# Kernel optimization log

Hardware: AMD Instinct MI355X
Metric: run time of the kernel (lower is better)

Reference implementation:

```python
import jax, jax.numpy as jnp
import numpy as np

DIM, HID, BATCH = 64, 512, 8192


def setup_inputs() -> dict:
    key = jax.random.key(0)
    ks = jax.random.split(key, 6)
    s1 = 1.0 / np.sqrt(DIM + 1)
    s2 = 1.0 / np.sqrt(HID)
    return {
        "t": jax.random.uniform(ks[0], (1,), dtype=jnp.float32),
        "x": jax.random.normal(ks[1], (BATCH, DIM), dtype=jnp.float32),
        "W1": jax.random.normal(ks[2], (DIM + 1, HID), dtype=jnp.float32) * s1,
        "b1": jnp.zeros((HID,), jnp.float32),
        "W2": jax.random.normal(ks[3], (HID, HID), dtype=jnp.float32) * s2,
        "b2": jnp.zeros((HID,), jnp.float32),
        "W3": jax.random.normal(ks[4], (HID, DIM), dtype=jnp.float32) * s2,
        "b3": jnp.zeros((DIM,), jnp.float32),
    }


def _vf_single(ts, xs, W1, b1, W2, b2, W3, b3):
    # xs: [dim], ts: scalar. Time concatenated as extra input feature.
    h = jnp.concatenate([xs, ts[None]])          # [dim+1]
    h = jnp.tanh(h @ W1 + b1)                    # [hid]
    h = jnp.tanh(h @ W2 + b2)                    # [hid]
    return h @ W3 + b3                           # [dim]


def reference(t, x, W1, b1, W2, b2, W3, b3):
    ts = t[0]
    vf = lambda xs: _vf_single(ts, xs, W1, b1, W2, b2, W3, b3)
    v = jax.vmap(vf)(x)                                   # [B, dim]
    # Exact divergence: trace of per-sample Jacobian dv/dx.
    # (Replaces the torch per-dim autograd.grad loop with one batched jacfwd.)
    J = jax.vmap(jax.jacfwd(vf))(x)                       # [B, dim, dim]
    div = jnp.trace(J, axis1=-2, axis2=-1)                # [B]
    return (v, -div[:, None])
```

## Files before the change

kernel.cpp:

```cpp
#include <hip/hip_runtime.h>

#define DIM 64
#define HID 512
#define BATCH 8192
#define MB 32
#define NTHR 1024

typedef __attribute__((ext_vector_type(8))) short short8;
typedef __attribute__((ext_vector_type(4))) float f32x4;
typedef __attribute__((ext_vector_type(16))) float f32x16;
typedef float float4_ __attribute__((ext_vector_type(4)));
typedef unsigned long long ull;

#define Z16 {0.f,0.f,0.f,0.f,0.f,0.f,0.f,0.f,0.f,0.f,0.f,0.f,0.f,0.f,0.f,0.f}

union U8 { short8 s8; unsigned short u[8]; };
union U4 { ull v; unsigned short u[4]; };

__device__ __forceinline__ unsigned short f2bf(float f) {
    union { float f; unsigned u; } v; v.f = f;
    return (unsigned short)((v.u + 0x7FFFu + ((v.u >> 16) & 1u)) >> 16);
}
__device__ __forceinline__ float tanh_fast(float x) {
    float e = __expf(2.f * x);
    return 1.f - __fdividef(2.f, e + 1.f);
}

__global__ __launch_bounds__(256) void prep(
        const float* __restrict__ t,  const float* __restrict__ W1,
        const float* __restrict__ b1, const float* __restrict__ W2,
        const float* __restrict__ W3,
        unsigned short* __restrict__ w2pk, unsigned short* __restrict__ ppk,
        unsigned short* __restrict__ w3pk, unsigned short* __restrict__ w1pk,
        float* __restrict__ c1) {
    __shared__ float w3sT[DIM * 33];
    __shared__ float w1s[DIM * DIM];
    int b = blockIdx.x;
    if (b >= 288) {
        int n = (b - 288) * 256 + threadIdx.x;
        c1[n] = fmaf(t[0], W1[DIM * HID + n], b1[n]);
        return;
    }
    int gid = b * 256 + threadIdx.x;
    int f = gid >> 6, l = gid & 63;
    if (f < 512) {
        int nt = f >> 5, ks = f & 31;
        int n = nt * 32 + (l & 31), k0 = ks * 16 + (l >> 5) * 8;
        unsigned short* o = w2pk + (size_t)(f * 64 + l) * 8;
#pragma unroll
        for (int e = 0; e < 8; ++e) o[e] = f2bf(W2[(size_t)(k0 + e) * HID + n]);
    } else if (f < 1024) {
        int ntb = (b * 4 - 512) >> 5;
        int jb  = (((b - 128) * 4) & 31) * 16;
        for (int idx = threadIdx.x; idx < 32 * DIM; idx += 256) {
            int dn = idx >> 6, i = idx & 63;
            w3sT[i * 33 + dn] = W3[(size_t)(ntb * 32 + dn) * DIM + i];
        }
        for (int idx = threadIdx.x; idx < DIM * DIM; idx += 256) {
            int i = idx >> 6, jj = idx & 63;
            w1s[i * DIM + jj] = W1[(size_t)i * HID + jb + jj];
        }
        __syncthreads();
        int fi = f - 512;
        int ks = fi & 31;
        int dn = l & 31, k0 = ks * 16 + (l >> 5) * 8;
        int n = ntb * 32 + dn;
        int jo = k0 - jb;
        float m[8] = {0.f,0.f,0.f,0.f,0.f,0.f,0.f,0.f};
#pragma unroll
        for (int i = 0; i < DIM; ++i) {
            float w3 = w3sT[i * 33 + dn];
            const float* wrow = &w1s[i * DIM + jo];
#pragma unroll
            for (int e = 0; e < 8; ++e) m[e] = fmaf(wrow[e], w3, m[e]);
        }
        unsigned short* o = ppk + (size_t)(fi * 64 + l) * 8;
#pragma unroll
        for (int e = 0; e < 8; ++e) o[e] = f2bf(W2[(size_t)(k0 + e) * HID + n] * m[e]);
    } else if (f < 1088) {
        int fi = f - 1024;
        int nt = fi >> 4, ks = fi & 15;
        int n = nt * 16 + (l & 15), k0 = ks * 32 + (l >> 4) * 8;
        unsigned short* o = w3pk + (size_t)(fi * 64 + l) * 8;
#pragma unroll
        for (int e = 0; e < 8; ++e) o[e] = f2bf(W3[(size_t)(k0 + e) * DIM + n]);
    } else {
        int fi = f - 1088;
        int nt = fi >> 1, ks = fi & 1;
        int n = nt * 16 + (l & 15), k0 = ks * 32 + (l >> 4) * 8;
        unsigned short* o = w1pk + (size_t)(fi * 64 + l) * 8;
#pragma unroll
        for (int e = 0; e < 8; ++e) o[e] = f2bf(W1[(size_t)(k0 + e) * HID + n]);
    }
}

__device__ __forceinline__ int act_addr(int sample, int colbyte) {
    return (sample * 1024 + colbyte) ^ ((sample & 15) << 4);
}

__global__ __launch_bounds__(NTHR)
__attribute__((amdgpu_waves_per_eu(4, 4)))
void fused_main(
        const float* __restrict__ x,  const float* __restrict__ c1,
        const float* __restrict__ b2, const float* __restrict__ b3,
        const unsigned short* __restrict__ w1pk, const unsigned short* __restrict__ w2pk,
        const unsigned short* __restrict__ ppk,  const unsigned short* __restrict__ w3pk,
        float* __restrict__ out) {
    __shared__ unsigned short h1s[MB * HID];
    __shared__ unsigned short d1s[MB * HID];
    __shared__ unsigned short h2s[MB * HID];
    __shared__ float wred[16][MB];
    char* h1b = (char*)h1s; char* d1b = (char*)d1s; char* h2b = (char*)h2s;

    const int tid = threadIdx.x, w = tid >> 6, l = tid & 63;
    const int lr = l & 15, g = l >> 4;
    const int s0 = blockIdx.x * MB;

    short8 xf[2][2];
#pragma unroll
    for (int nt = 0; nt < 2; ++nt)
#pragma unroll
        for (int ks = 0; ks < 2; ++ks) {
            const float* xp = x + (size_t)(s0 + nt * 16 + lr) * DIM + ks * 32 + g * 8;
            float4_ x0 = *(const float4_*)xp;
            float4_ x1 = *(const float4_*)(xp + 4);
            U8 u;
            u.u[0]=f2bf(x0.x); u.u[1]=f2bf(x0.y); u.u[2]=f2bf(x0.z); u.u[3]=f2bf(x0.w);
            u.u[4]=f2bf(x1.x); u.u[5]=f2bf(x1.y); u.u[6]=f2bf(x1.z); u.u[7]=f2bf(x1.w);
            xf[nt][ks] = u.s8;
        }
#pragma unroll
    for (int mi = 0; mi < 2; ++mi) {
        int mt = w * 2 + mi;
        short8 a0 = ((const short8*)w1pk)[(size_t)((mt * 2 + 0) * 64 + l)];
        short8 a1 = ((const short8*)w1pk)[(size_t)((mt * 2 + 1) * 64 + l)];
        float c1q[4];
#pragma unroll
        for (int r = 0; r < 4; ++r) c1q[r] = c1[mt * 16 + g * 4 + r];
#pragma unroll
        for (int nt = 0; nt < 2; ++nt) {
            f32x4 acc = {0.f, 0.f, 0.f, 0.f};
            acc = __builtin_amdgcn_mfma_f32_16x16x32_bf16(a0, xf[nt][0], acc, 0, 0, 0);
            acc = __builtin_amdgcn_mfma_f32_16x16x32_bf16(a1, xf[nt][1], acc, 0, 0, 0);
            int sample = nt * 16 + lr;
            U4 hu, du;
#pragma unroll
            for (int r = 0; r < 4; ++r) {
                float h = tanh_fast(acc[r] + c1q[r]);
                hu.u[r] = f2bf(h);
                du.u[r] = f2bf(fmaf(-h, h, 1.f));
            }
            int ab = act_addr(sample, (mt * 16 + g * 4) * 2);
            *(ull*)(h1b + ab) = hu.v;
            *(ull*)(d1b + ab) = du.v;
        }
    }
    __syncthreads();

    const short8* bw = (const short8*)w2pk + (size_t)(w * 32) * 64 + l;
    const short8* bp = (const short8*)ppk  + (size_t)(w * 32) * 64 + l;
    f32x16 z = Z16, s = Z16;
#pragma unroll 4
    for (int ks = 0; ks < 32; ++ks) {
        int ab = act_addr(l & 31, ks * 32 + (l >> 5) * 16);
        short8 ah = *(const short8*)(h1b + ab);
        short8 ad = *(const short8*)(d1b + ab);
        short8 bwv = bw[ks * 64];
        short8 bpv = bp[ks * 64];
        z = __builtin_amdgcn_mfma_f32_32x32x16_bf16(ah, bwv, z, 0, 0, 0);
        s = __builtin_amdgcn_mfma_f32_32x32x16_bf16(ad, bpv, s, 0, 0, 0);
    }

    float divp[16];
    {
        int c = w * 32 + (l & 31);
        float b2v = b2[c];
#pragma unroll
        for (int r = 0; r < 16; ++r) {
            int row = (r & 3) + 8 * (r >> 2) + 4 * (l >> 5);
            float h2 = tanh_fast(z[r] + b2v);
            float d2 = fmaf(-h2, h2, 1.f);
            divp[r] = s[r] * d2;
            *(unsigned short*)(h2b + act_addr(row, c * 2)) = f2bf(h2);
        }
    }
#pragma unroll
    for (int off = 1; off < 32; off <<= 1) {
#pragma unroll
        for (int r = 0; r < 16; ++r) divp[r] += __shfl_xor(divp[r], off, 64);
    }
    if ((l & 31) == 0) {
#pragma unroll
        for (int r = 0; r < 16; ++r) {
            int row = (r & 3) + 8 * (r >> 2) + 4 * (l >> 5);
            wred[w][row] = divp[r];
        }
    }
    __syncthreads();
    if (tid < MB) {
        float d = 0.f;
#pragma unroll
        for (int ww = 0; ww < 16; ++ww) d += wred[ww][tid];
        out[(size_t)BATCH * DIM + s0 + tid] = -d;
    }

    if (w < 8) {
        const int wm3 = w & 1, wn3 = w >> 1;
        f32x4 acc = {0.f, 0.f, 0.f, 0.f};
        const short8* W3f = (const short8*)w3pk + (size_t)(wn3 * 16) * 64 + l;
#pragma unroll
        for (int ks = 0; ks < 16; ++ks) {
            int ab = act_addr(wm3 * 16 + lr, ks * 64 + g * 16);
            short8 ah = *(const short8*)(h2b + ab);
            acc = __builtin_amdgcn_mfma_f32_16x16x32_bf16(ah, W3f[ks * 64], acc, 0, 0, 0);
        }
        int c = wn3 * 16 + lr;
        float b3v = b3[c];
#pragma unroll
        for (int r = 0; r < 4; ++r)
            out[(size_t)(s0 + wm3 * 16 + g * 4 + r) * DIM + c] = acc[r] + b3v;
    }
}

extern "C" void kernel_launch(void* const* d_in, const int* in_sizes, int n_in,
                              void* d_out, int out_size, void* d_ws, size_t ws_size,
                              hipStream_t stream) {
    const float* t  = (const float*)d_in[0];
    const float* x  = (const float*)d_in[1];
    const float* W1 = (const float*)d_in[2];
    const float* b1 = (const float*)d_in[3];
    const float* W2 = (const float*)d_in[4];
    const float* b2 = (const float*)d_in[5];
    const float* W3 = (const float*)d_in[6];
    const float* b3 = (const float*)d_in[7];
    float* out = (float*)d_out;

    char* ws = (char*)d_ws;
    unsigned short* w2pk = (unsigned short*)ws;
    unsigned short* ppk  = (unsigned short*)(ws + (512 << 10));
    unsigned short* w3pk = (unsigned short*)(ws + (1 << 20));
    unsigned short* w1pk = (unsigned short*)(ws + (1 << 20) + (64 << 10));
    float*          c1   = (float*)(ws + (1 << 20) + (128 << 10));

    prep<<<290, 256, 0, stream>>>(t, W1, b1, W2, W3, w2pk, ppk, w3pk, w1pk, c1);
    fused_main<<<BATCH / MB, NTHR, 0, stream>>>(x, c1, b2, b3, w1pk, w2pk, ppk, w3pk, out);
}
```

Measured before the change: 35.66 us.

## Split layer-2 waves into forward and tangent roles sharing A fragment

Instead of each of 16 waves computing both the forward z and tangent s GEMMs for one 32-column slice, waves 0-7 compute forward z for two column slices and waves 8-15 compute tangent s for two slices, reusing one A fragment load per step. Tangent waves then read back bf16 h2 from shared memory to form the divergence, while forward waves run the W3 output GEMM concurrently with that reduction. This halves the per-wave A-operand LDS reads and overlaps the divergence and output stages, but it uses bf16-rounded h2 for the derivative and adds a barrier.

```diff
diff --git a/kernel.cpp b/kernel.cpp
--- a/kernel.cpp
+++ b/kernel.cpp
@@ -16,10 +16,14 @@
 
 union U8 { short8 s8; unsigned short u[8]; };
 union U4 { ull v; unsigned short u[4]; };
+union FB { unsigned u; float f; };
 
 __device__ __forceinline__ unsigned short f2bf(float f) {
     union { float f; unsigned u; } v; v.f = f;
     return (unsigned short)((v.u + 0x7FFFu + ((v.u >> 16) & 1u)) >> 16);
+}
+__device__ __forceinline__ float bf2f(unsigned short b) {
+    FB v; v.u = (unsigned)b << 16; return v.f;
 }
 __device__ __forceinline__ float tanh_fast(float x) {
     float e = __expf(2.f * x);
@@ -109,7 +113,7 @@
     __shared__ unsigned short h1s[MB * HID];
     __shared__ unsigned short d1s[MB * HID];
     __shared__ unsigned short h2s[MB * HID];
-    __shared__ float wred[16][MB];
+    __shared__ float wred[8][MB];
     char* h1b = (char*)h1s; char* d1b = (char*)d1s; char* h2b = (char*)h2s;
 
     const int tid = threadIdx.x, w = tid >> 6, l = tid & 63;
@@ -157,54 +161,66 @@
     }
     __syncthreads();
 
-    const short8* bw = (const short8*)w2pk + (size_t)(w * 32) * 64 + l;
-    const short8* bp = (const short8*)ppk  + (size_t)(w * 32) * 64 + l;
-    f32x16 z = Z16, s = Z16;
+    const int q = w & 7, role = w >> 3;
+    const short8* Bf = (const short8*)(role ? ppk : w2pk);
+    const char* Ab = role ? d1b : h1b;
+    const short8* b0p = Bf + (size_t)((2 * q + 0) * 32) * 64 + l;
+    const short8* b1p = Bf + (size_t)((2 * q + 1) * 32) * 64 + l;
+    f32x16 a0 = Z16, a1 = Z16;
 #pragma unroll 4
     for (int ks = 0; ks < 32; ++ks) {
         int ab = act_addr(l & 31, ks * 32 + (l >> 5) * 16);
-        short8 ah = *(const short8*)(h1b + ab);
-        short8 ad = *(const short8*)(d1b + ab);
-        short8 bwv = bw[ks * 64];
-        short8 bpv = bp[ks * 64];
-        z = __builtin_amdgcn_mfma_f32_32x32x16_bf16(ah, bwv, z, 0, 0, 0);
-        s = __builtin_amdgcn_mfma_f32_32x32x16_bf16(ad, bpv, s, 0, 0, 0);
-    }
-
-    float divp[16];
-    {
-        int c = w * 32 + (l & 31);
-        float b2v = b2[c];
-#pragma unroll
-        for (int r = 0; r < 16; ++r) {
-            int row = (r & 3) + 8 * (r >> 2) + 4 * (l >> 5);
-            float h2 = tanh_fast(z[r] + b2v);
-            float d2 = fmaf(-h2, h2, 1.f);
-            divp[r] = s[r] * d2;
-            *(unsigned short*)(h2b + act_addr(row, c * 2)) = f2bf(h2);
-        }
-    }
-#pragma unroll
-    for (int off = 1; off < 32; off <<= 1) {
-#pragma unroll
-        for (int r = 0; r < 16; ++r) divp[r] += __shfl_xor(divp[r], off, 64);
-    }
-    if ((l & 31) == 0) {
-#pragma unroll
-        for (int r = 0; r < 16; ++r) {
-            int row = (r & 3) + 8 * (r >> 2) + 4 * (l >> 5);
-            wred[w][row] = divp[r];
+        short8 av  = *(const short8*)(Ab + ab);
+        short8 b0v = b0p[ks * 64];
+        short8 b1v = b1p[ks * 64];
+        a0 = __builtin_amdgcn_mfma_f32_32x32x16_bf16(av, b0v, a0, 0, 0, 0);
+        a1 = __builtin_amdgcn_mfma_f32_32x32x16_bf16(av, b1v, a1, 0, 0, 0);
+    }
+
+    if (role == 0) {
+#pragma unroll
+        for (int j = 0; j < 2; ++j) {
+            int c = (2 * q + j) * 32 + (l & 31);
+            float b2v = b2[c];
+            f32x16 acc = j ? a1 : a0;
+#pragma unroll
+            for (int r = 0; r < 16; ++r) {
+                int row = (r & 3) + 8 * (r >> 2) + 4 * (l >> 5);
+                float h2 = tanh_fast(acc[r] + b2v);
+                *(unsigned short*)(h2b + act_addr(row, c * 2)) = f2bf(h2);
+            }
         }
     }
     __syncthreads();
-    if (tid < MB) {
-        float d = 0.f;
-#pragma unroll
-        for (int ww = 0; ww < 16; ++ww) d += wred[ww][tid];
-        out[(size_t)BATCH * DIM + s0 + tid] = -d;
-    }
-
-    if (w < 8) {
+
+    if (role == 1) {
+        float divp[16];
+#pragma unroll
+        for (int r = 0; r < 16; ++r) divp[r] = 0.f;
+#pragma unroll
+        for (int j = 0; j < 2; ++j) {
+            int c = (2 * q + j) * 32 + (l & 31);
+            f32x16 acc = j ? a1 : a0;
+#pragma unroll
+            for (int r = 0; r < 16; ++r) {
+                int row = (r & 3) + 8 * (r >> 2) + 4 * (l >> 5);
+                float h2 = bf2f(*(const unsigned short*)(h2b + act_addr(row, c * 2)));
+                divp[r] = fmaf(acc[r], fmaf(-h2, h2, 1.f), divp[r]);
+            }
+        }
+#pragma unroll
+        for (int off = 1; off < 32; off <<= 1) {
+#pragma unroll
+            for (int r = 0; r < 16; ++r) divp[r] += __shfl_xor(divp[r], off, 64);
+        }
+        if ((l & 31) == 0) {
+#pragma unroll
+            for (int r = 0; r < 16; ++r) {
+                int row = (r & 3) + 8 * (r >> 2) + 4 * (l >> 5);
+                wred[q][row] = divp[r];
+            }
+        }
+    } else {
         const int wm3 = w & 1, wn3 = w >> 1;
         f32x4 acc = {0.f, 0.f, 0.f, 0.f};
         const short8* W3f = (const short8*)w3pk + (size_t)(wn3 * 16) * 64 + l;
@@ -219,6 +235,13 @@
 #pragma unroll
         for (int r = 0; r < 4; ++r)
             out[(size_t)(s0 + wm3 * 16 + g * 4 + r) * DIM + c] = acc[r] + b3v;
+    }
+    __syncthreads();
+    if (tid < MB) {
+        float d = 0.f;
+#pragma unroll
+        for (int ww = 0; ww < 8; ++ww) d += wred[ww][tid];
+        out[(size_t)BATCH * DIM + s0 + tid] = -d;
     }
 }
 
```

After: 33.20 us. 1.07x faster.

## Split fused MLP kernel into separate forward and divergence kernels

Applied to the files above, without the earlier changes.

Splits the single fused kernel into two launches. The first computes the forward pass, writes v, and saves h2 as a bf16 image to global workspace. The second recomputes layer 1 to get the tanh derivative, runs the P-weighted GEMM, reloads h2 and reduces the divergence. This halves the accumulators and shared memory per kernel so more blocks can be resident, at the cost of an extra launch, redundant layer-1 work and an 8 MB global round trip.

```diff
diff --git a/kernel.cpp b/kernel.cpp
--- a/kernel.cpp
+++ b/kernel.cpp
@@ -16,10 +16,14 @@
 
 union U8 { short8 s8; unsigned short u[8]; };
 union U4 { ull v; unsigned short u[4]; };
+union FB { unsigned u; float f; };
 
 __device__ __forceinline__ unsigned short f2bf(float f) {
     union { float f; unsigned u; } v; v.f = f;
     return (unsigned short)((v.u + 0x7FFFu + ((v.u >> 16) & 1u)) >> 16);
+}
+__device__ __forceinline__ float bf2f(unsigned short b) {
+    FB v; v.u = (unsigned)b << 16; return v.f;
 }
 __device__ __forceinline__ float tanh_fast(float x) {
     float e = __expf(2.f * x);
@@ -98,24 +102,12 @@
     return (sample * 1024 + colbyte) ^ ((sample & 15) << 4);
 }
 
-__global__ __launch_bounds__(NTHR)
-__attribute__((amdgpu_waves_per_eu(4, 4)))
-void fused_main(
-        const float* __restrict__ x,  const float* __restrict__ c1,
-        const float* __restrict__ b2, const float* __restrict__ b3,
-        const unsigned short* __restrict__ w1pk, const unsigned short* __restrict__ w2pk,
-        const unsigned short* __restrict__ ppk,  const unsigned short* __restrict__ w3pk,
-        float* __restrict__ out) {
-    __shared__ unsigned short h1s[MB * HID];
-    __shared__ unsigned short d1s[MB * HID];
-    __shared__ unsigned short h2s[MB * HID];
-    __shared__ float wred[16][MB];
-    char* h1b = (char*)h1s; char* d1b = (char*)d1s; char* h2b = (char*)h2s;
-
-    const int tid = threadIdx.x, w = tid >> 6, l = tid & 63;
+template <int STORE_D>
+__device__ __forceinline__ void phase1(
+        const float* __restrict__ x, const float* __restrict__ c1,
+        const unsigned short* __restrict__ w1pk,
+        char* dstb, int s0, int w, int l) {
     const int lr = l & 15, g = l >> 4;
-    const int s0 = blockIdx.x * MB;
-
     short8 xf[2][2];
 #pragma unroll
     for (int nt = 0; nt < 2; ++nt)
@@ -143,66 +135,50 @@
             acc = __builtin_amdgcn_mfma_f32_16x16x32_bf16(a0, xf[nt][0], acc, 0, 0, 0);
             acc = __builtin_amdgcn_mfma_f32_16x16x32_bf16(a1, xf[nt][1], acc, 0, 0, 0);
             int sample = nt * 16 + lr;
-            U4 hu, du;
+            U4 u;
 #pragma unroll
             for (int r = 0; r < 4; ++r) {
                 float h = tanh_fast(acc[r] + c1q[r]);
-                hu.u[r] = f2bf(h);
-                du.u[r] = f2bf(fmaf(-h, h, 1.f));
+                u.u[r] = STORE_D ? f2bf(fmaf(-h, h, 1.f)) : f2bf(h);
             }
-            int ab = act_addr(sample, (mt * 16 + g * 4) * 2);
-            *(ull*)(h1b + ab) = hu.v;
-            *(ull*)(d1b + ab) = du.v;
-        }
-    }
-    __syncthreads();
-
-    const short8* bw = (const short8*)w2pk + (size_t)(w * 32) * 64 + l;
-    const short8* bp = (const short8*)ppk  + (size_t)(w * 32) * 64 + l;
-    f32x16 z = Z16, s = Z16;
+            *(ull*)(dstb + act_addr(sample, (mt * 16 + g * 4) * 2)) = u.v;
+        }
+    }
+}
+
+__global__ __launch_bounds__(NTHR, 4) void zmain(
+        const float* __restrict__ x,  const float* __restrict__ c1,
+        const float* __restrict__ b2, const float* __restrict__ b3,
+        const unsigned short* __restrict__ w1pk, const unsigned short* __restrict__ w2pk,
+        const unsigned short* __restrict__ w3pk,
+        unsigned short* __restrict__ h2img, float* __restrict__ out) {
+    __shared__ unsigned short h1s[MB * HID];
+    __shared__ unsigned short h2s[MB * HID];
+    char* h1b = (char*)h1s; char* h2b = (char*)h2s;
+    const int tid = threadIdx.x, w = tid >> 6, l = tid & 63;
+    const int lr = l & 15, g = l >> 4;
+    const int s0 = blockIdx.x * MB;
+
+    phase1<0>(x, c1, w1pk, h1b, s0, w, l);
+    __syncthreads();
+
+    const short8* bwp = (const short8*)w2pk + (size_t)(w * 32) * 64 + l;
+    f32x16 z = Z16;
 #pragma unroll 4
     for (int ks = 0; ks < 32; ++ks) {
-        int ab = act_addr(l & 31, ks * 32 + (l >> 5) * 16);
-        short8 ah = *(const short8*)(h1b + ab);
-        short8 ad = *(const short8*)(d1b + ab);
-        short8 bwv = bw[ks * 64];
-        short8 bpv = bp[ks * 64];
-        z = __builtin_amdgcn_mfma_f32_32x32x16_bf16(ah, bwv, z, 0, 0, 0);
-        s = __builtin_amdgcn_mfma_f32_32x32x16_bf16(ad, bpv, s, 0, 0, 0);
-    }
-
-    float divp[16];
+        short8 av = *(const short8*)(h1b + act_addr(l & 31, ks * 32 + (l >> 5) * 16));
+        z = __builtin_amdgcn_mfma_f32_32x32x16_bf16(av, bwp[ks * 64], z, 0, 0, 0);
+    }
     {
         int c = w * 32 + (l & 31);
         float b2v = b2[c];
 #pragma unroll
         for (int r = 0; r < 16; ++r) {
             int row = (r & 3) + 8 * (r >> 2) + 4 * (l >> 5);
-            float h2 = tanh_fast(z[r] + b2v);
-            float d2 = fmaf(-h2, h2, 1.f);
-            divp[r] = s[r] * d2;
-            *(unsigned short*)(h2b + act_addr(row, c * 2)) = f2bf(h2);
-        }
-    }
-#pragma unroll
-    for (int off = 1; off < 32; off <<= 1) {
-#pragma unroll
-        for (int r = 0; r < 16; ++r) divp[r] += __shfl_xor(divp[r], off, 64);
-    }
-    if ((l & 31) == 0) {
-#pragma unroll
-        for (int r = 0; r < 16; ++r) {
-            int row = (r & 3) + 8 * (r >> 2) + 4 * (l >> 5);
-            wred[w][row] = divp[r];
-        }
-    }
-    __syncthreads();
-    if (tid < MB) {
-        float d = 0.f;
-#pragma unroll
-        for (int ww = 0; ww < 16; ++ww) d += wred[ww][tid];
-        out[(size_t)BATCH * DIM + s0 + tid] = -d;
-    }
+            *(unsigned short*)(h2b + act_addr(row, c * 2)) = f2bf(tanh_fast(z[r] + b2v));
+        }
+    }
+    __syncthreads();
 
     if (w < 8) {
         const int wm3 = w & 1, wn3 = w >> 1;
@@ -210,8 +186,7 @@
         const short8* W3f = (const short8*)w3pk + (size_t)(wn3 * 16) * 64 + l;
 #pragma unroll
         for (int ks = 0; ks < 16; ++ks) {
-            int ab = act_addr(wm3 * 16 + lr, ks * 64 + g * 16);
-            short8 ah = *(const short8*)(h2b + ab);
+            short8 ah = *(const short8*)(h2b + act_addr(wm3 * 16 + lr, ks * 64 + g * 16));
             acc = __builtin_amdgcn_mfma_f32_16x16x32_bf16(ah, W3f[ks * 64], acc, 0, 0, 0);
         }
         int c = wn3 * 16 + lr;
@@ -219,6 +194,71 @@
 #pragma unroll
         for (int r = 0; r < 4; ++r)
             out[(size_t)(s0 + wm3 * 16 + g * 4 + r) * DIM + c] = acc[r] + b3v;
+    } else {
+        int tsrc = tid - 512;
+        float4_* dst = (float4_*)(h2img + (size_t)blockIdx.x * MB * HID);
+        const float4_* s4 = (const float4_*)h2s;
+#pragma unroll
+        for (int k = 0; k < 4; ++k) dst[tsrc * 4 + k] = s4[tsrc * 4 + k];
+    }
+}
+
+__global__ __launch_bounds__(NTHR, 4) void smain(
+        const float* __restrict__ x,  const float* __restrict__ c1,
+        const unsigned short* __restrict__ w1pk, const unsigned short* __restrict__ ppk,
+        const unsigned short* __restrict__ h2img, float* __restrict__ out) {
+    __shared__ unsigned short d1s[MB * HID];
+    __shared__ unsigned short h2l[MB * HID];
+    __shared__ float wred[16][MB];
+    char* d1b = (char*)d1s; char* h2b = (char*)h2l;
+    const int tid = threadIdx.x, w = tid >> 6, l = tid & 63;
+    const int s0 = blockIdx.x * MB;
+
+    phase1<1>(x, c1, w1pk, d1b, s0, w, l);
+    const float4_* src = (const float4_*)(h2img + (size_t)blockIdx.x * MB * HID);
+    float4_ hv0 = src[tid * 2 + 0];
+    float4_ hv1 = src[tid * 2 + 1];
+    __syncthreads();
+
+    const short8* bpp = (const short8*)ppk + (size_t)(w * 32) * 64 + l;
+    f32x16 s = Z16;
+#pragma unroll 4
+    for (int ks = 0; ks < 32; ++ks) {
+        short8 av = *(const short8*)(d1b + act_addr(l & 31, ks * 32 + (l >> 5) * 16));
+        s = __builtin_amdgcn_mfma_f32_32x32x16_bf16(av, bpp[ks * 64], s, 0, 0, 0);
+    }
+    ((float4_*)h2l)[tid * 2 + 0] = hv0;
+    ((float4_*)h2l)[tid * 2 + 1] = hv1;
+    __syncthreads();
+
+    float divp[16];
+    {
+        int c = w * 32 + (l & 31);
+#pragma unroll
+        for (int r = 0; r < 16; ++r) {
+            int row = (r & 3) + 8 * (r >> 2) + 4 * (l >> 5);
+            float h2 = bf2f(*(const unsigned short*)(h2b + act_addr(row, c * 2)));
+            divp[r] = s[r] * fmaf(-h2, h2, 1.f);
+        }
+    }
+#pragma unroll
+    for (int off = 1; off < 32; off <<= 1) {
+#pragma unroll
+        for (int r = 0; r < 16; ++r) divp[r] += __shfl_xor(divp[r], off, 64);
+    }
+    if ((l & 31) == 0) {
+#pragma unroll
+        for (int r = 0; r < 16; ++r) {
+            int row = (r & 3) + 8 * (r >> 2) + 4 * (l >> 5);
+            wred[w][row] = divp[r];
+        }
+    }
+    __syncthreads();
+    if (tid < MB) {
+        float d = 0.f;
+#pragma unroll
+        for (int ww = 0; ww < 16; ++ww) d += wred[ww][tid];
+        out[(size_t)BATCH * DIM + s0 + tid] = -d;
     }
 }
 
@@ -236,12 +276,14 @@
     float* out = (float*)d_out;
 
     char* ws = (char*)d_ws;
-    unsigned short* w2pk = (unsigned short*)ws;
-    unsigned short* ppk  = (unsigned short*)(ws + (512 << 10));
-    unsigned short* w3pk = (unsigned short*)(ws + (1 << 20));
-    unsigned short* w1pk = (unsigned short*)(ws + (1 << 20) + (64 << 10));
-    float*          c1   = (float*)(ws + (1 << 20) + (128 << 10));
-
-    prep<<<290, 256, 0, stream>>>(t, W1, b1, W2, W3, w2pk, ppk, w3pk, w1pk, c1);
-    fused_main<<<BATCH / MB, NTHR, 0, stream>>>(x, c1, b2, b3, w1pk, w2pk, ppk, w3pk, out);
-}
+    unsigned short* w2pk  = (unsigned short*)ws;
+    unsigned short* ppk   = (unsigned short*)(ws + (512 << 10));
+    unsigned short* w3pk  = (unsigned short*)(ws + (1 << 20));
+    unsigned short* w1pk  = (unsigned short*)(ws + (1 << 20) + (64 << 10));
+    float*          c1    = (float*)(ws + (1 << 20) + (128 << 10));
+    unsigned short* h2img = (unsigned short*)(ws + (1 << 20) + (192 << 10));
+
+    prep <<<290, 256, 0, stream>>>(t, W1, b1, W2, W3, w2pk, ppk, w3pk, w1pk, c1);
+    zmain<<<BATCH / MB, NTHR, 0, stream>>>(x, c1, b2, b3, w1pk, w2pk, w3pk, h2img, out);
+    smain<<<BATCH / MB, NTHR, 0, stream>>>(x, c1, w1pk, ppk, h2img, out);
+}
```

After: 48.04 us. 1.35x slower.

## Rotate per-block weight tile and k order, split W2 and P loops, drop waves_per_eu

Applied to the files above, without the earlier changes.

Each block now starts at a different W2/P column tile (warp index offset by block id) and a rotated k-step order in both the layer-2 and layer-3 loops. The aim is to spread concurrent blocks across different weight cache lines instead of all hitting the same addresses together. The fused z/s MFMA loop is split into two sequential loops, and the waves_per_eu(4,4) attribute is removed. This changes register pressure and the instruction interleaving, and the rotated indexing adds some address arithmetic.

```diff
diff --git a/kernel.cpp b/kernel.cpp
--- a/kernel.cpp
+++ b/kernel.cpp
@@ -16,6 +16,7 @@
 
 union U8 { short8 s8; unsigned short u[8]; };
 union U4 { ull v; unsigned short u[4]; };
+union FB { unsigned u; float f; };
 
 __device__ __forceinline__ unsigned short f2bf(float f) {
     union { float f; unsigned u; } v; v.f = f;
@@ -98,9 +99,7 @@
     return (sample * 1024 + colbyte) ^ ((sample & 15) << 4);
 }
 
-__global__ __launch_bounds__(NTHR)
-__attribute__((amdgpu_waves_per_eu(4, 4)))
-void fused_main(
+__global__ __launch_bounds__(NTHR) void fused_main(
         const float* __restrict__ x,  const float* __restrict__ c1,
         const float* __restrict__ b2, const float* __restrict__ b3,
         const unsigned short* __restrict__ w1pk, const unsigned short* __restrict__ w2pk,
@@ -114,7 +113,8 @@
 
     const int tid = threadIdx.x, w = tid >> 6, l = tid & 63;
     const int lr = l & 15, g = l >> 4;
-    const int s0 = blockIdx.x * MB;
+    const int bid = blockIdx.x;
+    const int s0 = bid * MB;
 
     short8 xf[2][2];
 #pragma unroll
@@ -157,31 +157,36 @@
     }
     __syncthreads();
 
-    const short8* bw = (const short8*)w2pk + (size_t)(w * 32) * 64 + l;
-    const short8* bp = (const short8*)ppk  + (size_t)(w * 32) * 64 + l;
-    f32x16 z = Z16, s = Z16;
+    const int q2 = (w + bid) & 15;
+    const int rot = (bid * 5) & 31;
+    const short8* bwp = (const short8*)w2pk + (size_t)(q2 * 32) * 64 + l;
+    const short8* bpp = (const short8*)ppk  + (size_t)(q2 * 32) * 64 + l;
+
+    f32x16 zacc = Z16;
 #pragma unroll 4
-    for (int ks = 0; ks < 32; ++ks) {
-        int ab = act_addr(l & 31, ks * 32 + (l >> 5) * 16);
-        short8 ah = *(const short8*)(h1b + ab);
-        short8 ad = *(const short8*)(d1b + ab);
-        short8 bwv = bw[ks * 64];
-        short8 bpv = bp[ks * 64];
-        z = __builtin_amdgcn_mfma_f32_32x32x16_bf16(ah, bwv, z, 0, 0, 0);
-        s = __builtin_amdgcn_mfma_f32_32x32x16_bf16(ad, bpv, s, 0, 0, 0);
+    for (int i = 0; i < 32; ++i) {
+        int ks = (i + rot) & 31;
+        short8 av = *(const short8*)(h1b + act_addr(l & 31, ks * 32 + (l >> 5) * 16));
+        zacc = __builtin_amdgcn_mfma_f32_32x32x16_bf16(av, bwp[ks * 64], zacc, 0, 0, 0);
+    }
+    f32x16 sacc = Z16;
+#pragma unroll 4
+    for (int i = 0; i < 32; ++i) {
+        int ks = (i + rot) & 31;
+        short8 ad = *(const short8*)(d1b + act_addr(l & 31, ks * 32 + (l >> 5) * 16));
+        sacc = __builtin_amdgcn_mfma_f32_32x32x16_bf16(ad, bpp[ks * 64], sacc, 0, 0, 0);
     }
 
     float divp[16];
     {
-        int c = w * 32 + (l & 31);
+        int c = q2 * 32 + (l & 31);
         float b2v = b2[c];
 #pragma unroll
         for (int r = 0; r < 16; ++r) {
             int row = (r & 3) + 8 * (r >> 2) + 4 * (l >> 5);
-            float h2 = tanh_fast(z[r] + b2v);
-            float d2 = fmaf(-h2, h2, 1.f);
-            divp[r] = s[r] * d2;
+            float h2 = tanh_fast(zacc[r] + b2v);
             *(unsigned short*)(h2b + act_addr(row, c * 2)) = f2bf(h2);
+            divp[r] = sacc[r] * fmaf(-h2, h2, 1.f);
         }
     }
 #pragma unroll
@@ -197,28 +202,29 @@
         }
     }
     __syncthreads();
+
+    if (w < 8) {
+        const int wm3 = w & 1, wn3 = w >> 1;
+        const int rot3 = (bid * 3) & 15;
+        f32x4 acc = {0.f, 0.f, 0.f, 0.f};
+        const short8* W3f = (const short8*)w3pk + (size_t)(wn3 * 16) * 64 + l;
+#pragma unroll
+        for (int i = 0; i < 16; ++i) {
+            int ks = (i + rot3) & 15;
+            short8 ah = *(const short8*)(h2b + act_addr(wm3 * 16 + lr, ks * 64 + g * 16));
+            acc = __builtin_amdgcn_mfma_f32_16x16x32_bf16(ah, W3f[ks * 64], acc, 0, 0, 0);
+        }
+        int c = wn3 * 16 + lr;
+        float b3v = b3[c];
+#pragma unroll
+        for (int r = 0; r < 4; ++r)
+            out[(size_t)(s0 + wm3 * 16 + g * 4 + r) * DIM + c] = acc[r] + b3v;
+    }
     if (tid < MB) {
         float d = 0.f;
 #pragma unroll
         for (int ww = 0; ww < 16; ++ww) d += wred[ww][tid];
         out[(size_t)BATCH * DIM + s0 + tid] = -d;
-    }
-
-    if (w < 8) {
-        const int wm3 = w & 1, wn3 = w >> 1;
-        f32x4 acc = {0.f, 0.f, 0.f, 0.f};
-        const short8* W3f = (const short8*)w3pk + (size_t)(wn3 * 16) * 64 + l;
-#pragma unroll
-        for (int ks = 0; ks < 16; ++ks) {
-            int ab = act_addr(wm3 * 16 + lr, ks * 64 + g * 16);
-            short8 ah = *(const short8*)(h2b + ab);
-            acc = __builtin_amdgcn_mfma_f32_16x16x32_bf16(ah, W3f[ks * 64], acc, 0, 0, 0);
-        }
-        int c = wn3 * 16 + lr;
-        float b3v = b3[c];
-#pragma unroll
-        for (int r = 0; r < 4; ++r)
-            out[(size_t)(s0 + wm3 * 16 + g * 4 + r) * DIM + c] = acc[r] + b3v;
     }
 }
 
```

Result: faster. 32.86 us (-7.9%).
